# Optimization experiments

Hardware: AMD Instinct MI355X
Metric: run time of the kernel (lower is better)

## Reference

```python
import jax, jax.numpy as jnp
import numpy as np
from jax import lax

TWN_THRESHOLD_FACTOR = 0.05


def ternary_quantize(w, t):
    # codes in {-1, 0, +1}
    return (w > t).astype(w.dtype) - (w < -t).astype(w.dtype)


def setup_inputs() -> dict:
    key = jax.random.key(0)
    kx, kw, kb = jax.random.split(key, 3)
    x = jax.random.normal(kx, (32, 128, 56, 56), dtype=jnp.float32)
    weight = jax.random.normal(kw, (256, 128, 3, 3), dtype=jnp.float32)
    bias = jax.random.normal(kb, (256,), dtype=jnp.float32)
    return {"x": x, "weight": weight, "bias": bias}


def reference(x, weight, bias):
    # threshold from detached weights (matches weight.detach().abs().max())
    threshold = TWN_THRESHOLD_FACTOR * jnp.max(jnp.abs(lax.stop_gradient(weight)))
    q_weight = ternary_quantize(weight, threshold)
    out = lax.conv_general_dilated(
        x, q_weight,
        window_strides=(1, 1),
        padding="VALID",  # F.conv2d default padding=0
        dimension_numbers=("NCHW", "OIHW", "NCHW"),
    )
    return out + bias[None, :, None, None]
```

## Files before the change

### kernel.cpp

```cpp
#include <hip/hip_runtime.h>
#include <hip/hip_bf16.h>
#include <stdint.h>

#define NB   32
#define CIN  128
#define HIN  56
#define WIN  56
#define KOUT 256
#define HOUT 54
#define WOUT 54
#define PQ   (HOUT*WOUT)
#define NPIX (NB*PQ)
#define KK   (CIN*9)
#define HW   (HIN*WIN)
#define TWN_FACTOR 0.05f

typedef short bf16x8 __attribute__((ext_vector_type(8)));
typedef float f32x4  __attribute__((ext_vector_type(4)));

__device__ __forceinline__ void glds16(const void* g, void* l) {
  __builtin_amdgcn_global_load_lds(
      (__attribute__((address_space(1))) void*)(g),
      (__attribute__((address_space(3))) void*)(l),
      16, 0, 0);
}

__global__ void prep_k(const float* __restrict__ x, const float4* __restrict__ w4,
                       float* __restrict__ amax, __hip_bfloat16* __restrict__ xt) {
  __shared__ __hip_bfloat16 tl[64 * 130 + 32];
  __shared__ float sm[4];
  int bid = blockIdx.x;
  int t   = threadIdx.x;

  if (bid < 288) {
    float4 v = w4[bid * 256 + t];
    float m = fmaxf(fmaxf(fabsf(v.x), fabsf(v.y)), fmaxf(fabsf(v.z), fabsf(v.w)));
    #pragma unroll
    for (int off = 32; off > 0; off >>= 1)
      m = fmaxf(m, __shfl_down(m, off));
    int lane = t & 63, wv = t >> 6;
    if (lane == 0) sm[wv] = m;
    __syncthreads();
    if (t == 0)
      atomicMax(amax, fmaxf(fmaxf(sm[0], sm[1]), fmaxf(sm[2], sm[3])));
    return;
  }

  int b2 = bid - 288;
  int n  = b2 / 49, pc = b2 - n * 49;
  const float* xb = x + (size_t)n * CIN * HW + pc * 64;
  int f4 = t & 15, c0 = t >> 4;
  #pragma unroll
  for (int rd = 0; rd < 8; ++rd) {
    int c = c0 + rd * 16;
    float4 v = *(const float4*)(xb + (size_t)c * HW + f4 * 4);
    tl[(f4 * 4 + 0) * 130 + c] = __float2bfloat16(v.x);
    tl[(f4 * 4 + 1) * 130 + c] = __float2bfloat16(v.y);
    tl[(f4 * 4 + 2) * 130 + c] = __float2bfloat16(v.z);
    tl[(f4 * 4 + 3) * 130 + c] = __float2bfloat16(v.w);
  }
  __syncthreads();
  int cc = t & 15, p0 = t >> 4;
  __hip_bfloat16* op = xt + ((size_t)n * HW + pc * 64) * CIN + cc * 8;
  #pragma unroll
  for (int p = p0; p < 64; p += 16)
    *(bf16x8*)(op + (size_t)p * CIN) = *(const bf16x8*)&tl[p * 130 + cc * 8];
}

__global__ void quant_k(const float* __restrict__ w, const float* __restrict__ amax,
                        __hip_bfloat16* __restrict__ qA) {
  float thr = TWN_FACTOR * (*amax);
  int t  = blockIdx.x * 256 + threadIdx.x;
  int kc = t >> 8, row = t & 255;
  int rs = kc >> 4, c0 = (kc & 15) << 3;
  bf16x8 q;
  #pragma unroll
  for (int j = 0; j < 8; ++j) {
    float v  = w[(size_t)(row * CIN + c0 + j) * 9 + rs];
    float qq = (v > thr) ? 1.f : ((v < -thr) ? -1.f : 0.f);
    q[j] = (short)__bfloat16_as_ushort(__float2bfloat16(qq));
  }
  *(bf16x8*)(qA + (size_t)t * 8) = q;
}

__global__ __launch_bounds__(256, 3) void conv_gemm(
    const __hip_bfloat16* __restrict__ xt,
    const __hip_bfloat16* __restrict__ qA,
    const float* __restrict__ bias,
    float* __restrict__ out) {
  __shared__ __hip_bfloat16 Bs[3][128 * 64];

  const int tid  = threadIdx.x;
  const int wave = tid >> 6;
  const int lane = tid & 63;
  const int quad = lane >> 4;
  const int l16  = lane & 15;

  const int orig = blockIdx.x;
  const int xcd  = orig & 7;
  const int loc  = orig >> 3;
  const int bid  = (xcd < 2) ? xcd * 183 + loc
                             : 366 + (xcd - 2) * 182 + loc;

  const int ktile = bid & 1;
  const int ptile = bid >> 1;
  const int k0    = ktile * 128;
  const int pbase = ptile * 128;

  const int wm = (wave >> 1) * 64;
  const int wn = (wave & 1) * 64;

  const int r8 = lane >> 3;
  const int ch = lane & 7;
  unsigned boffm[4];
  #pragma unroll
  for (int m = 0; m < 4; ++m) {
    int row  = wave * 32 + m * 8 + r8;
    int prow = pbase + row;
    int n = prow / PQ; int rm = prow - n * PQ;
    int p = rm / WOUT; int q = rm - p * WOUT;
    boffm[m] = (unsigned)(n * HW + p * WIN + q) * CIN + ((ch ^ (row & 7)) << 3);
  }

  unsigned aoff[4];
  #pragma unroll
  for (int i = 0; i < 4; ++i)
    aoff[i] = (unsigned)(quad * 256 + (k0 + wm + i * 16 + l16)) * 8;

  f32x4 acc[4][4];
  #pragma unroll
  for (int i = 0; i < 4; ++i)
    #pragma unroll
    for (int j = 0; j < 4; ++j)
      acc[i][j] = (f32x4){0.f, 0.f, 0.f, 0.f};

  {
    char* bdst0 = (char*)Bs + wave * 4096;
    #pragma unroll
    for (int m = 0; m < 4; ++m)
      glds16(xt + boffm[m], bdst0 + m * 1024);
    char* bdst1 = (char*)Bs + 16384 + wave * 4096;
    #pragma unroll
    for (int m = 0; m < 4; ++m)
      glds16(xt + boffm[m] + 64u, bdst1 + m * 1024);
  }

  #pragma unroll
  for (int t = 0; t < 18; ++t) {
    asm volatile("s_waitcnt vmcnt(4)" ::: "memory");
    __builtin_amdgcn_s_barrier();
    __builtin_amdgcn_sched_barrier(0);

    const unsigned astep = ((unsigned)(t >> 1) * 16 + (unsigned)(t & 1) * 8) * 2048;

    bf16x8 af[2][4];
    #pragma unroll
    for (int h = 0; h < 2; ++h)
      #pragma unroll
      for (int i = 0; i < 4; ++i)
        af[h][i] = *(const bf16x8*)(qA + aoff[i] + astep + (unsigned)h * 4 * 2048);
    __builtin_amdgcn_sched_barrier(0);

    if (t < 16) {
      const int tn  = t + 2;
      const int rsn = tn >> 1;
      const int rn  = rsn / 3, sn = rsn - rn * 3;
      const unsigned bst = (unsigned)((rn * WIN + sn) * CIN + (tn & 1) * 64);
      char* bdst = (char*)Bs + (unsigned)(tn % 3) * 16384 + wave * 4096;
      #pragma unroll
      for (int m = 0; m < 4; ++m)
        glds16(xt + boffm[m] + bst, bdst + m * 1024);
    }

    const char* bp = (const char*)Bs + (unsigned)(t % 3) * 16384;
    #pragma unroll
    for (int h = 0; h < 2; ++h) {
      bf16x8 bfr[4];
      #pragma unroll
      for (int i = 0; i < 4; ++i) {
        int row = wn + i * 16 + l16;
        bfr[i] = *(const bf16x8*)(bp + (row * 64 + (((h * 4 + quad) ^ (row & 7)) << 3)) * 2);
      }
      #pragma unroll
      for (int i = 0; i < 4; ++i)
        #pragma unroll
        for (int j = 0; j < 4; ++j)
          acc[i][j] = __builtin_amdgcn_mfma_f32_16x16x32_bf16(af[h][i], bfr[j], acc[i][j], 0, 0, 0);
    }
  }

  __syncthreads();

  {
    float* Sw = (float*)Bs + wave * 2048;
    const int ST  = 65;
    const int rk  = lane >> 3;
    const int rp  = (lane & 7) * 4;
    const float4* b4 = (const float4*)bias;

    #pragma unroll
    for (int i = 0; i < 4; ++i) {
      float4 bv = b4[(k0 + wm + i * 16 + quad * 4) >> 2];
      #pragma unroll
      for (int j = 0; j < 4; ++j) {
        Sw[(quad * 4 + 0) * ST + j * 16 + l16] = acc[i][j][0] + bv.x;
        Sw[(quad * 4 + 1) * ST + j * 16 + l16] = acc[i][j][1] + bv.y;
        Sw[(quad * 4 + 2) * ST + j * 16 + l16] = acc[i][j][2] + bv.z;
        Sw[(quad * 4 + 3) * ST + j * 16 + l16] = acc[i][j][3] + bv.w;
      }
      asm volatile("s_waitcnt lgkmcnt(0)" ::: "memory");
      __builtin_amdgcn_sched_barrier(0);
      #pragma unroll
      for (int ri = 0; ri < 2; ++ri) {
        int klocal = ri * 8 + rk;
        int k = k0 + wm + i * 16 + klocal;
        #pragma unroll
        for (int cg = 0; cg < 2; ++cg) {
          int pixl = cg * 32 + rp;
          float4 v = *(const float4*)&Sw[klocal * ST + pixl];
          int pix = pbase + wn + pixl;
          int n = pix / PQ, pq = pix - n * PQ;
          *(float4*)(out + (size_t)n * (KOUT * PQ) + (size_t)k * PQ + pq) = v;
        }
      }
      asm volatile("s_waitcnt lgkmcnt(0)" ::: "memory");
      __builtin_amdgcn_sched_barrier(0);
    }
  }
}

extern "C" void kernel_launch(void* const* d_in, const int* in_sizes, int n_in,
                              void* d_out, int out_size, void* d_ws, size_t ws_size,
                              hipStream_t stream) {
  const float* x    = (const float*)d_in[0];
  const float* w    = (const float*)d_in[1];
  const float* bias = (const float*)d_in[2];
  float* out = (float*)d_out;

  float* amax = (float*)d_ws;
  __hip_bfloat16* xt = (__hip_bfloat16*)((char*)d_ws + 256);
  __hip_bfloat16* qA = (__hip_bfloat16*)((char*)d_ws + 256 + (size_t)NB * HW * CIN * 2);

  prep_k  <<<dim3(1856), dim3(256), 0, stream>>>(x, (const float4*)w, amax, xt);
  quant_k <<<dim3(144),  dim3(256), 0, stream>>>(w, amax, qA);
  conv_gemm<<<dim3(1458), dim3(256), 0, stream>>>(xt, qA, bias, out);
}
```

Baseline: 196.2 us.

## Double-buffer A fragments in registers and pack channel pairs in prep transpose

The conv GEMM now loads the quantized-weight A fragments for the next k-step into a second register set during the current step. Previously it loaded them at the top of each step right before the MFMAs needed them, exposing global-load latency. The waitcnt accounting is adjusted so the last step drains all loads, and the MFMA blocks are wrapped in s_setprio to favour the issuing wave. The prep transpose also converts two channels at a time and writes them to LDS as packed 32-bit stores, halving the number of LDS writes. The cost is doubled A-fragment register usage, which risks pressure under the 3-blocks-per-SIMD launch bound.

```diff
diff --git a/kernel.cpp b/kernel.cpp
--- a/kernel.cpp
+++ b/kernel.cpp
@@ -25,6 +25,11 @@
       16, 0, 0);
 }
 
+__device__ __forceinline__ unsigned pack_bf16(float a, float b) {
+  return (unsigned)__bfloat16_as_ushort(__float2bfloat16(a)) |
+         ((unsigned)__bfloat16_as_ushort(__float2bfloat16(b)) << 16);
+}
+
 __global__ void prep_k(const float* __restrict__ x, const float4* __restrict__ w4,
                        float* __restrict__ amax, __hip_bfloat16* __restrict__ xt) {
   __shared__ __hip_bfloat16 tl[64 * 130 + 32];
@@ -49,15 +54,18 @@
   int b2 = bid - 288;
   int n  = b2 / 49, pc = b2 - n * 49;
   const float* xb = x + (size_t)n * CIN * HW + pc * 64;
-  int f4 = t & 15, c0 = t >> 4;
-  #pragma unroll
-  for (int rd = 0; rd < 8; ++rd) {
-    int c = c0 + rd * 16;
-    float4 v = *(const float4*)(xb + (size_t)c * HW + f4 * 4);
-    tl[(f4 * 4 + 0) * 130 + c] = __float2bfloat16(v.x);
-    tl[(f4 * 4 + 1) * 130 + c] = __float2bfloat16(v.y);
-    tl[(f4 * 4 + 2) * 130 + c] = __float2bfloat16(v.z);
-    tl[(f4 * 4 + 3) * 130 + c] = __float2bfloat16(v.w);
+  int f4  = t & 15;
+  int cp0 = t >> 4;
+  #pragma unroll
+  for (int rd = 0; rd < 4; ++rd) {
+    int cp = cp0 + rd * 16;
+    const float* s0 = xb + (size_t)(2 * cp) * HW + f4 * 4;
+    float4 v0 = *(const float4*)(s0);
+    float4 v1 = *(const float4*)(s0 + HW);
+    *(unsigned*)&tl[(f4 * 4 + 0) * 130 + 2 * cp] = pack_bf16(v0.x, v1.x);
+    *(unsigned*)&tl[(f4 * 4 + 1) * 130 + 2 * cp] = pack_bf16(v0.y, v1.y);
+    *(unsigned*)&tl[(f4 * 4 + 2) * 130 + 2 * cp] = pack_bf16(v0.z, v1.z);
+    *(unsigned*)&tl[(f4 * 4 + 3) * 130 + 2 * cp] = pack_bf16(v0.w, v1.w);
   }
   __syncthreads();
   int cc = t & 15, p0 = t >> 4;
@@ -134,11 +142,20 @@
     for (int j = 0; j < 4; ++j)
       acc[i][j] = (f32x4){0.f, 0.f, 0.f, 0.f};
 
+  bf16x8 af[2][8];
+
   {
     char* bdst0 = (char*)Bs + wave * 4096;
     #pragma unroll
     for (int m = 0; m < 4; ++m)
       glds16(xt + boffm[m], bdst0 + m * 1024);
+    __builtin_amdgcn_sched_barrier(0);
+    #pragma unroll
+    for (int h = 0; h < 2; ++h)
+      #pragma unroll
+      for (int i = 0; i < 4; ++i)
+        af[0][h * 4 + i] = *(const bf16x8*)(qA + aoff[i] + (unsigned)h * 4 * 2048);
+    __builtin_amdgcn_sched_barrier(0);
     char* bdst1 = (char*)Bs + 16384 + wave * 4096;
     #pragma unroll
     for (int m = 0; m < 4; ++m)
@@ -147,18 +164,21 @@
 
   #pragma unroll
   for (int t = 0; t < 18; ++t) {
-    asm volatile("s_waitcnt vmcnt(4)" ::: "memory");
+    if (t < 17) asm volatile("s_waitcnt vmcnt(4)" ::: "memory");
+    else        asm volatile("s_waitcnt vmcnt(0)" ::: "memory");
     __builtin_amdgcn_s_barrier();
     __builtin_amdgcn_sched_barrier(0);
 
-    const unsigned astep = ((unsigned)(t >> 1) * 16 + (unsigned)(t & 1) * 8) * 2048;
-
-    bf16x8 af[2][4];
-    #pragma unroll
-    for (int h = 0; h < 2; ++h)
-      #pragma unroll
-      for (int i = 0; i < 4; ++i)
-        af[h][i] = *(const bf16x8*)(qA + aoff[i] + astep + (unsigned)h * 4 * 2048);
+    if (t < 17) {
+      const int tn = t + 1;
+      const unsigned astep = ((unsigned)(tn >> 1) * 16 + (unsigned)(tn & 1) * 8) * 2048;
+      #pragma unroll
+      for (int h = 0; h < 2; ++h)
+        #pragma unroll
+        for (int i = 0; i < 4; ++i)
+          af[tn & 1][h * 4 + i] =
+              *(const bf16x8*)(qA + aoff[i] + astep + (unsigned)h * 4 * 2048);
+    }
     __builtin_amdgcn_sched_barrier(0);
 
     if (t < 16) {
@@ -171,6 +191,7 @@
       for (int m = 0; m < 4; ++m)
         glds16(xt + boffm[m] + bst, bdst + m * 1024);
     }
+    __builtin_amdgcn_sched_barrier(0);
 
     const char* bp = (const char*)Bs + (unsigned)(t % 3) * 16384;
     #pragma unroll
@@ -181,11 +202,14 @@
         int row = wn + i * 16 + l16;
         bfr[i] = *(const bf16x8*)(bp + (row * 64 + (((h * 4 + quad) ^ (row & 7)) << 3)) * 2);
       }
+      __builtin_amdgcn_s_setprio(1);
       #pragma unroll
       for (int i = 0; i < 4; ++i)
         #pragma unroll
         for (int j = 0; j < 4; ++j)
-          acc[i][j] = __builtin_amdgcn_mfma_f32_16x16x32_bf16(af[h][i], bfr[j], acc[i][j], 0, 0, 0);
+          acc[i][j] = __builtin_amdgcn_mfma_f32_16x16x32_bf16(af[t & 1][h * 4 + i], bfr[j],
+                                                              acc[i][j], 0, 0, 0);
+      __builtin_amdgcn_s_setprio(0);
     }
   }
 
```

New measurement: 199.2 us. Within noise of the previous version (+1.5%).
